# Performance work log

Hardware: AMD Instinct MI355X
Metric: run time of the kernel (lower is better)

## Reference

```python
import jax, jax.numpy as jnp
import numpy as np

B, N, IN_F, E, H, A = 8, 1024, 1024, 256, 4, 64
ALPHA = 0.2          # leaky relu slope
NEG = -9e15          # mask value from original code


def setup_inputs() -> dict:
    key = jax.random.key(0)
    k = jax.random.split(key, 7)
    x = jax.random.normal(k[0], (B * N, IN_F), dtype=jnp.float32)
    adj = jax.random.randint(k[1], (B, N, N), 0, 2, dtype=jnp.int32)
    # per-head GAT params: W (H, IN_F, E); a split into a1, a2 (H, E) each,
    # since cat([Wh_i, Wh_j]) @ a == Wh_i @ a1 + Wh_j @ a2 exactly.
    W = jax.random.normal(k[2], (H, IN_F, E), dtype=jnp.float32) * 0.05
    a1 = jax.random.normal(k[3], (H, E), dtype=jnp.float32) * 0.05
    a2 = jax.random.normal(k[4], (H, E), dtype=jnp.float32) * 0.05
    W_act = jax.random.normal(k[5], (H * E, A), dtype=jnp.float32) * 0.05
    b_act = jnp.zeros((A,), dtype=jnp.float32)
    return {"x": x, "adj": adj, "W": W, "a1": a1, "a2": a2,
            "W_act": W_act, "b_act": b_act}


def reference(x, adj, W, a1, a2, W_act, b_act):
    b, n, _ = adj.shape
    xr = x.reshape(b, n, -1)                                   # (B, N, IN_F)
    Wh = jnp.einsum('bni,hio->hbno', xr, W)                    # (H, B, N, E)
    f1 = jnp.einsum('hbno,ho->hbn', Wh, a1)                    # a . Wh_i part
    f2 = jnp.einsum('hbno,ho->hbn', Wh, a2)                    # a . Wh_j part
    e = jax.nn.leaky_relu(f1[..., :, None] + f2[..., None, :], ALPHA)  # (H,B,N,N)
    e = jnp.where(adj[None] > 0, e, NEG)
    att = jax.nn.softmax(e, axis=-1)                           # masked softmax
    h_prime = jnp.einsum('hbnm,hbmo->hbno', att, Wh)           # (H, B, N, E)
    h_prime = jax.nn.elu(h_prime)                              # concat=True -> elu
    feat = jnp.transpose(h_prime, (1, 2, 0, 3)).reshape(b * n, H * E)
    return feat @ W_act + b_act                                # (B*N, A)
```

## Files before the change

kernel.cpp:

```cpp
#include <hip/hip_runtime.h>
#include <stdint.h>

typedef __attribute__((ext_vector_type(8))) short short8;
typedef __attribute__((ext_vector_type(4))) float f32x4;
typedef __attribute__((ext_vector_type(16))) float f32x16;


__device__ __forceinline__ float b2f(unsigned short u) {
    union { unsigned int i; float f; } v; v.i = ((unsigned int)u) << 16; return v.f;
}
__device__ __forceinline__ unsigned short f2b(float f) {
    union { float f; unsigned int i; } v; v.f = f;
    unsigned int u = v.i;
    u = (u + 0x7FFFu + ((u >> 16) & 1u)) >> 16;
    return (unsigned short)u;
}
__device__ __forceinline__ unsigned int cvtpk(float a, float b) {
    unsigned int r;
    asm("v_cvt_pk_bf16_f32 %0, %1, %2" : "=v"(r) : "v"(a), "v"(b));
    return r;
}
__device__ __forceinline__ float blo(unsigned int u) {
    union { unsigned int i; float f; } v; v.i = u << 16; return v.f;
}
__device__ __forceinline__ float bhi(unsigned int u) {
    union { unsigned int i; float f; } v; v.i = u & 0xFFFF0000u; return v.f;
}
__device__ __forceinline__ void glds16(const void* g, const void* l) {
    __builtin_amdgcn_global_load_lds(
        (const __attribute__((address_space(1))) unsigned int*)g,
        (__attribute__((address_space(3))) unsigned int*)l, 16, 0, 0);
}

__device__ __forceinline__ void cvt8(const void* in, unsigned short* out,
                                     int f, int grp) {
    if (f) {
        ((ushort4*)out)[grp * 2]     = ((const ushort4*)in)[grp * 2];
        ((ushort4*)out)[grp * 2 + 1] = ((const ushort4*)in)[grp * 2 + 1];
    } else {
        const float4* p = (const float4*)in + (size_t)grp * 2;
        float4 a = p[0], b = p[1];
        ushort4 o0, o1;
        o0.x = f2b(a.x); o0.y = f2b(a.y); o0.z = f2b(a.z); o0.w = f2b(a.w);
        o1.x = f2b(b.x); o1.y = f2b(b.y); o1.z = f2b(b.z); o1.w = f2b(b.w);
        ((ushort4*)out)[grp * 2]     = o0;
        ((ushort4*)out)[grp * 2 + 1] = o1;
    }
}

__global__ __launch_bounds__(256) void prep_all(
        const unsigned int* __restrict__ x4,
        const void* __restrict__ x, const void* __restrict__ W,
        const void* __restrict__ Wact,
        const void* __restrict__ a1, const void* __restrict__ a2,
        const void* __restrict__ bact,
        unsigned short* __restrict__ xb, unsigned short* __restrict__ WT,
        unsigned short* __restrict__ WactT,
        unsigned short* __restrict__ a1b, unsigned short* __restrict__ a2b,
        unsigned short* __restrict__ bactb,
        int* __restrict__ flag, float4* __restrict__ fz) {
    __shared__ unsigned int tile[64 * 65];
    __shared__ int sflag;
    int tid = threadIdx.x;
    int bid = blockIdx.x;
    if (bid >= 4352 && bid < 4416) {
        fz[(bid - 4352) * 256 + tid] = float4{0.f, 0.f, 0.f, 0.f};
        return;
    }
    if (tid < 64) {
        unsigned int wv = x4[tid];
        unsigned int e = (wv >> 7) & 0xFF;
        unsigned long long m = __ballot(e >= 100 && e <= 140);
        if (tid == 0) sflag = (__popcll(m) >= 48) ? 1 : 0;
    }
    __syncthreads();
    int f = sflag;

    if (bid < 4096) {
        cvt8(x, xb, f, bid * 256 + tid);
        return;
    }
    if (bid == 4416) {
        if (tid == 0) flag[0] = f;
        if (tid < 128) cvt8(a1, a1b, f, tid);
        else           cvt8(a2, a2b, f, tid - 128);
        if (tid < 8)   cvt8(bact, bactb, f, tid);
        return;
    }
    const void* in; unsigned short* out; int C, bt, c0, r0;
    if (bid < 4352) {
        int lb = bid - 4096;
        in = W; out = WT; C = 256;
        c0 = (lb & 3) * 64;
        r0 = ((lb >> 2) & 15) * 64;
        bt = lb >> 6;
    } else {
        int lb = bid - 4417;
        in = Wact; out = WactT; C = 64;
        c0 = 0; r0 = lb * 64; bt = 0;
    }
    int rl = tid >> 2;
    int cc = (tid & 3) * 16;
    size_t ibase = ((size_t)bt * 1024 + (r0 + rl)) * C + c0 + cc;
    unsigned short v[16];
    if (f) {
        const unsigned short* p = (const unsigned short*)in + ibase;
        short8 a = *(const short8*)p;
        short8 b = *(const short8*)(p + 8);
#pragma unroll
        for (int j = 0; j < 8; j++) { v[j] = (unsigned short)a[j]; v[8 + j] = (unsigned short)b[j]; }
    } else {
        const float* p = (const float*)in + ibase;
#pragma unroll
        for (int j = 0; j < 16; j++) v[j] = f2b(p[j]);
    }
#pragma unroll
    for (int j = 0; j < 16; j++)
        tile[(cc + j) * 65 + rl] = v[j];
    __syncthreads();
    int cl = tid >> 2;
    int rch = (tid & 3) * 16;
    unsigned short o[16];
#pragma unroll
    for (int j = 0; j < 16; j++)
        o[j] = (unsigned short)tile[cl * 65 + rch + j];
    unsigned short* op = out + ((size_t)bt * C + (c0 + cl)) * 1024 + r0 + rch;
#pragma unroll
    for (int q = 0; q < 4; q++) {
        ushort4 s; s.x = o[q*4]; s.y = o[q*4+1]; s.z = o[q*4+2]; s.w = o[q*4+3];
        ((ushort4*)op)[q] = s;
    }
}

__global__ void pack_adj(const int* __restrict__ adj,
                         unsigned int* __restrict__ maskT) {
    int gid = blockIdx.x * 256 + threadIdx.x;
    int lane = threadIdx.x & 63;
    unsigned long long m = __ballot(adj[gid] > 0);
    if (lane == 0) {
        int lin = gid >> 6;
        int mw = (lin & 15) * 2;
        int bn = lin >> 4;
        int b = bn >> 10, n = bn & 1023;
        maskT[(size_t)(b * 32 + mw) * 1024 + n]     = (unsigned int)m;
        maskT[(size_t)(b * 32 + mw + 1) * 1024 + n] = (unsigned int)(m >> 32);
    }
}

__global__ __launch_bounds__(256) void k1_gemm(
        const unsigned short* __restrict__ x,
        const unsigned short* __restrict__ WT,
        unsigned short* __restrict__ WhF,
        const unsigned short* __restrict__ a1b,
        const unsigned short* __restrict__ a2b,
        float* __restrict__ f1, float* __restrict__ f2) {
    __shared__ unsigned short smA0[16 * 512];
    __shared__ unsigned short smA1[16 * 512];
    __shared__ unsigned short smB0[16 * 512];
    __shared__ unsigned short smB1[16 * 512];
    int tid = threadIdx.x;
    int w = tid >> 6, lane = tid & 63;
    int lr = lane & 15, lq = lane >> 4;
    int lin = blockIdx.x + 8 * blockIdx.y;
    int xcd = lin & 7, kk = lin >> 3;
    int ct = kk >> 3;
    int rt = xcd * 8 + (kk & 7);
    int col0 = ct * 128;
    int row0 = rt * 128;
    int h = col0 >> 8;
    int e_base = col0 & 255;
    int b = row0 >> 10;
    int m_base = row0 & 1023;
    int wr = w >> 1, wc = w & 1;

    f32x4 acc[4][4] = {};

    auto stage = [&](unsigned short* dA, unsigned short* dB, int k0) {
#pragma unroll
        for (int s = 0; s < 4; s++) {
            int g = 4 * w + s;
            int rb = g & 7, kh = g >> 3;
            const unsigned short* srcA =
                x + (size_t)(row0 + rb * 16 + lr) * 1024 + k0 + kh * 32 + lq * 8;
            glds16(srcA, dA + g * 512);
            const unsigned short* srcB =
                WT + (size_t)(h * 256 + e_base + rb * 16 + lr) * 1024
                   + k0 + kh * 32 + lq * 8;
            glds16(srcB, dB + g * 512);
        }
    };
    auto compute = [&](const unsigned short* sA, const unsigned short* sB) {
#pragma unroll
        for (int kh = 0; kh < 2; kh++) {
            short8 af[4], bf[4];
#pragma unroll
            for (int i = 0; i < 4; i++)
                af[i] = *(const short8*)&sA[(kh * 8 + wr * 4 + i) * 512 + lane * 8];
#pragma unroll
            for (int j = 0; j < 4; j++)
                bf[j] = *(const short8*)&sB[(kh * 8 + wc * 4 + j) * 512 + lane * 8];
#pragma unroll
            for (int i = 0; i < 4; i++)
#pragma unroll
                for (int j = 0; j < 4; j++)
                    acc[i][j] = __builtin_amdgcn_mfma_f32_16x16x32_bf16(
                        af[i], bf[j], acc[i][j], 0, 0, 0);
        }
    };

    stage(smA0, smB0, 0);
    __syncthreads();
    for (int t = 0; t < 16; t += 2) {
        stage(smA1, smB1, (t + 1) * 64);
        compute(smA0, smB0);
        __syncthreads();
        if (t + 2 < 16) stage(smA0, smB0, (t + 2) * 64);
        compute(smA1, smB1);
        __syncthreads();
    }

    int hb = h * 8 + b;
#pragma unroll
    for (int i = 0; i < 4; i++) {
#pragma unroll
        for (int j = 0; j < 4; j++) {
            int e = e_base + (wc * 4 + j) * 16 + lr;
            int et = e >> 5, e31 = e & 31;
            int m16 = (m_base >> 4) + wr * 4 + i;
            ushort4 vs;
            vs.x = f2b(acc[i][j][0]);
            vs.y = f2b(acc[i][j][1]);
            vs.z = f2b(acc[i][j][2]);
            vs.w = f2b(acc[i][j][3]);
            size_t idx = ((size_t)((hb * 8 + et) * 64 + m16) * 512)
                         + ((lq >> 1) * 32 + e31) * 8 + (lq & 1) * 4;
            *(ushort4*)&WhF[idx] = vs;
        }
    }

    const float LOG2E = 1.44269504f;
    float a1v[4], a2v[4];
#pragma unroll
    for (int j = 0; j < 4; j++) {
        int e = e_base + (wc * 4 + j) * 16 + lr;
        a1v[j] = b2f(a1b[h * 256 + e]);
        a2v[j] = b2f(a2b[h * 256 + e]);
    }
#pragma unroll
    for (int i = 0; i < 4; i++) {
#pragma unroll
        for (int reg = 0; reg < 4; reg++) {
            float s1 = 0.f, s2 = 0.f;
#pragma unroll
            for (int j = 0; j < 4; j++) {
                s1 += acc[i][j][reg] * a1v[j];
                s2 += acc[i][j][reg] * a2v[j];
            }
            s1 += __shfl_xor(s1, 1, 64); s2 += __shfl_xor(s2, 1, 64);
            s1 += __shfl_xor(s1, 2, 64); s2 += __shfl_xor(s2, 2, 64);
            s1 += __shfl_xor(s1, 4, 64); s2 += __shfl_xor(s2, 4, 64);
            s1 += __shfl_xor(s1, 8, 64); s2 += __shfl_xor(s2, 8, 64);
            if (lr == 0) {
                int m = m_base + (wr * 4 + i) * 16 + lq * 4 + reg;
                atomicAdd(&f1[hb * 1024 + m], s1 * LOG2E);
                atomicAdd(&f2[hb * 1024 + m], s2 * LOG2E);
            }
        }
    }
}

__global__ __launch_bounds__(512, 4) void k2_attn(
        const unsigned short* __restrict__ WhF,
        const unsigned int* __restrict__ maskT,
        const float* __restrict__ f1, const float* __restrict__ f2,
        unsigned short* __restrict__ feat) {
    __shared__ unsigned short ptile[2][2][32][40];
    __shared__ float dred[2][4][32];
    int tid = threadIdx.x;
    int w = tid >> 6, lane = tid & 63;
    int q = w & 3, wrg = w >> 2;
    int l5 = lane >> 5, l31 = lane & 31;
    int bid = blockIdx.x;
    int xcd = bid & 7, idx = bid >> 3;
    int hb = xcd + 8 * (idx >> 4);
    int rgb = idx & 15;
    int n0 = rgb * 64 + wrg * 32;
    int h = hb >> 3, b = hb & 7;
    int row = n0 + l31;
    float f1n = f1[hb * 1024 + row];
    const unsigned short* whb = WhF + (size_t)(hb * 8 + q * 2) * 64 * 512
                                + lane * 8;
    const unsigned int* mrow = maskT + (size_t)b * 32 * 1024 + row;
    const float* f2p = f2 + hb * 1024 + q * 8 + l5 * 4;
    int cshift = q * 8 + l5 * 4;

    f32x16 acc[2] = {};
    float den = 0.f;

    short8 bufA[2][2], bufB[2][2];
#pragma unroll
    for (int et = 0; et < 2; et++)
#pragma unroll
        for (int ks = 0; ks < 2; ks++)
            bufA[et][ks] = *(const short8*)(whb + (size_t)(et * 64 + ks) * 512);

    unsigned int mw = mrow[0];
    float4 fv = *(const float4*)f2p;

    for (int mb = 0; mb < 32; mb += 2) {
        {
            float fvv[4] = {fv.x, fv.y, fv.z, fv.w};
            unsigned int mloc = mw >> cshift;
            float pv[4];
#pragma unroll
            for (int j = 0; j < 4; j++) {
                float t_ = f1n + fvv[j];
                float e_ = fmaxf(t_, 0.2f * t_);
                pv[j] = ((mloc >> j) & 1u) ? exp2f(e_) : 0.f;
            }
            unsigned int r0 = cvtpk(pv[0], pv[1]);
            unsigned int r1 = cvtpk(pv[2], pv[3]);
            den += (blo(r0) + bhi(r0)) + (blo(r1) + bhi(r1));
            uint2 pr; pr.x = r0; pr.y = r1;
            *(uint2*)&ptile[0][wrg][l31][cshift] = pr;
            mw = mrow[(size_t)(mb + 1) * 1024];
            fv = *(const float4*)(f2p + (mb + 1) * 32);
            __syncthreads();
            short8 af0 = *(const short8*)&ptile[0][wrg][l31][l5 * 8];
            short8 af1 = *(const short8*)&ptile[0][wrg][l31][16 + l5 * 8];
            int m16n = (mb + 1) * 2;
#pragma unroll
            for (int et = 0; et < 2; et++)
#pragma unroll
                for (int ks = 0; ks < 2; ks++)
                    bufB[et][ks] =
                        *(const short8*)(whb + (size_t)(et * 64 + m16n + ks) * 512);
            __builtin_amdgcn_s_setprio(1);
#pragma unroll
            for (int et = 0; et < 2; et++) {
                acc[et] = __builtin_amdgcn_mfma_f32_32x32x16_bf16(
                    af0, bufA[et][0], acc[et], 0, 0, 0);
                acc[et] = __builtin_amdgcn_mfma_f32_32x32x16_bf16(
                    af1, bufA[et][1], acc[et], 0, 0, 0);
            }
            __builtin_amdgcn_s_setprio(0);
        }
        {
            float fvv[4] = {fv.x, fv.y, fv.z, fv.w};
            unsigned int mloc = mw >> cshift;
            float pv[4];
#pragma unroll
            for (int j = 0; j < 4; j++) {
                float t_ = f1n + fvv[j];
                float e_ = fmaxf(t_, 0.2f * t_);
                pv[j] = ((mloc >> j) & 1u) ? exp2f(e_) : 0.f;
            }
            unsigned int r0 = cvtpk(pv[0], pv[1]);
            unsigned int r1 = cvtpk(pv[2], pv[3]);
            den += (blo(r0) + bhi(r0)) + (blo(r1) + bhi(r1));
            uint2 pr; pr.x = r0; pr.y = r1;
            *(uint2*)&ptile[1][wrg][l31][cshift] = pr;
            if (mb < 30) {
                mw = mrow[(size_t)(mb + 2) * 1024];
                fv = *(const float4*)(f2p + (mb + 2) * 32);
            }
            __syncthreads();
            short8 af0 = *(const short8*)&ptile[1][wrg][l31][l5 * 8];
            short8 af1 = *(const short8*)&ptile[1][wrg][l31][16 + l5 * 8];
            if (mb < 30) {
                int m16n = (mb + 2) * 2;
#pragma unroll
                for (int et = 0; et < 2; et++)
#pragma unroll
                    for (int ks = 0; ks < 2; ks++)
                        bufA[et][ks] =
                            *(const short8*)(whb + (size_t)(et * 64 + m16n + ks) * 512);
            }
            __builtin_amdgcn_s_setprio(1);
#pragma unroll
            for (int et = 0; et < 2; et++) {
                acc[et] = __builtin_amdgcn_mfma_f32_32x32x16_bf16(
                    af0, bufB[et][0], acc[et], 0, 0, 0);
                acc[et] = __builtin_amdgcn_mfma_f32_32x32x16_bf16(
                    af1, bufB[et][1], acc[et], 0, 0, 0);
            }
            __builtin_amdgcn_s_setprio(0);
        }
    }

    den += __shfl_xor(den, 32, 64);
    if (l5 == 0) dred[wrg][q][l31] = den;
    __syncthreads();
    float denf = dred[wrg][0][l31] + dred[wrg][1][l31]
               + dred[wrg][2][l31] + dred[wrg][3][l31];

#pragma unroll
    for (int reg = 0; reg < 16; reg++) {
        int r = (reg & 3) + 8 * (reg >> 2) + 4 * l5;
        float dr = __shfl(denf, r, 64);
        float rdr = 1.0f / dr;
        int nn = n0 + r;
#pragma unroll
        for (int et = 0; et < 2; et++) {
            int e = q * 64 + et * 32 + l31;
            float v = acc[et][reg] * rdr;
            float o = v > 0.f ? v : __expf(v) - 1.f;
            feat[(size_t)(b * 1024 + nn) * 1024 + h * 256 + e] = f2b(o);
        }
    }
}

__global__ __launch_bounds__(256) void k3_out(
        const unsigned short* __restrict__ feat,
        const unsigned short* __restrict__ WactT,
        const unsigned short* __restrict__ bact,
        void* __restrict__ out, const int* __restrict__ flag) {
    __shared__ unsigned short sa0[2 * 512], sa1[2 * 512];
    __shared__ unsigned short sb0[4 * 512], sb1[4 * 512];
    int tid = threadIdx.x;
    int w = tid >> 6, lane = tid & 63;
    int lr = lane & 15, lq = lane >> 4;
    int row0 = blockIdx.x * 32;
    int g = w & 1, ch = w >> 1;
    int bf16out = *flag;
    f32x4 acc[2] = {};

    auto stage = [&](unsigned short* dA, unsigned short* dB, int k0) {
        if (w < 2) {
            const unsigned short* src =
                feat + (size_t)(row0 + w * 16 + lr) * 1024 + k0 + lq * 8;
            glds16(src, dA + w * 512);
        } else {
#pragma unroll
            for (int s = 0; s < 2; s++) {
                int t = (w - 2) * 2 + s;
                const unsigned short* src =
                    WactT + (size_t)(t * 16 + lr) * 1024 + k0 + lq * 8;
                glds16(src, dB + t * 512);
            }
        }
    };
    auto compute = [&](const unsigned short* sA, const unsigned short* sB) {
        short8 af = *(const short8*)&sA[g * 512 + lane * 8];
#pragma unroll
        for (int j = 0; j < 2; j++) {
            short8 bf = *(const short8*)&sB[(ch * 2 + j) * 512 + lane * 8];
            acc[j] = __builtin_amdgcn_mfma_f32_16x16x32_bf16(af, bf, acc[j], 0, 0, 0);
        }
    };

    stage(sa0, sb0, 0);
    __syncthreads();
    for (int t = 0; t < 32; t += 2) {
        stage(sa1, sb1, (t + 1) * 32);
        compute(sa0, sb0);
        __syncthreads();
        if (t + 2 < 32) stage(sa0, sb0, (t + 2) * 32);
        compute(sa1, sb1);
        __syncthreads();
    }
#pragma unroll
    for (int j = 0; j < 2; j++) {
        int col = ch * 32 + j * 16 + lr;
        float bv = b2f(bact[col]);
#pragma unroll
        for (int rr = 0; rr < 4; rr++) {
            int r = row0 + g * 16 + lq * 4 + rr;
            float val = acc[j][rr] + bv;
            if (bf16out) ((unsigned short*)out)[(size_t)r * 64 + col] = f2b(val);
            else         ((float*)out)[(size_t)r * 64 + col] = val;
        }
    }
}

extern "C" void kernel_launch(void* const* d_in, const int* in_sizes, int n_in,
                              void* d_out, int out_size, void* d_ws, size_t ws_size,
                              hipStream_t stream) {
    const void* x    = d_in[0];
    const int*  adj  = (const int*)d_in[1];
    const void* W    = d_in[2];
    const void* a1   = d_in[3];
    const void* a2   = d_in[4];
    const void* Wact = d_in[5];
    const void* bact = d_in[6];

    char* ws = (char*)d_ws;
    unsigned short* WhF   = (unsigned short*)(ws);
    unsigned short* xb    = (unsigned short*)(ws + 16777216);
    unsigned short* feat  = (unsigned short*)(ws + 16777216);
    unsigned short* WT    = (unsigned short*)(ws + 33554432);
    unsigned int*   maskT = (unsigned int*)(ws + 33554432);
    unsigned short* WactT = (unsigned short*)(ws + 35651584);
    float*          f1    = (float*)(ws + 35782656);
    float*          f2    = (float*)(ws + 35913728);
    unsigned short* a1b   = (unsigned short*)(ws + 36044800);
    unsigned short* a2b   = (unsigned short*)(ws + 36046848);
    unsigned short* bactb = (unsigned short*)(ws + 36048896);
    int*            flag  = (int*)(ws + 36049024);
    if (ws_size < (size_t)36049040) return;

    prep_all<<<4433, 256, 0, stream>>>((const unsigned int*)x, x, W, Wact,
                                       a1, a2, bact, xb, WT, WactT,
                                       a1b, a2b, bactb, flag, (float4*)f1);
    k1_gemm<<<dim3(8, 64), 256, 0, stream>>>(xb, WT, WhF, a1b, a2b, f1, f2);
    pack_adj<<<32768, 256, 0, stream>>>(adj, maskT);
    k2_attn<<<512, 512, 0, stream>>>(WhF, maskT, f1, f2, feat);
    k3_out<<<256, 256, 0, stream>>>(feat, WactT, bactb, d_out, flag);
}
```

Baseline: 200.9 us.

## Fuse adjacency mask packing into the prep kernel with per-wave row loops

```diff
diff --git a/kernel.cpp b/kernel.cpp
--- a/kernel.cpp
+++ b/kernel.cpp
@@ -54,15 +54,37 @@
         const void* __restrict__ Wact,
         const void* __restrict__ a1, const void* __restrict__ a2,
         const void* __restrict__ bact,
+        const int* __restrict__ adj,
         unsigned short* __restrict__ xb, unsigned short* __restrict__ WT,
         unsigned short* __restrict__ WactT,
         unsigned short* __restrict__ a1b, unsigned short* __restrict__ a2b,
         unsigned short* __restrict__ bactb,
-        int* __restrict__ flag, float4* __restrict__ fz) {
+        int* __restrict__ flag, float4* __restrict__ fz,
+        unsigned int* __restrict__ maskT) {
     __shared__ unsigned int tile[64 * 65];
     __shared__ int sflag;
     int tid = threadIdx.x;
     int bid = blockIdx.x;
+    if (bid >= 4433) {
+        int lb = bid - 4433;
+        int w = tid >> 6, lane = tid & 63;
+#pragma unroll 1
+        for (int rr = 0; rr < 16; rr++) {
+            int gr = lb * 64 + w * 16 + rr;
+            int b = gr >> 10, n = gr & 1023;
+            const int* rowp = adj + (size_t)gr * 1024 + lane;
+            unsigned int* mp = maskT + (size_t)b * 32 * 1024 + n;
+#pragma unroll
+            for (int k = 0; k < 16; k++) {
+                unsigned long long m = __ballot(rowp[k * 64] > 0);
+                if (lane == 0) {
+                    mp[(size_t)(k * 2) * 1024]     = (unsigned int)m;
+                    mp[(size_t)(k * 2 + 1) * 1024] = (unsigned int)(m >> 32);
+                }
+            }
+        }
+        return;
+    }
     if (bid >= 4352 && bid < 4416) {
         fz[(bid - 4352) * 256 + tid] = float4{0.f, 0.f, 0.f, 0.f};
         return;
@@ -129,21 +151,6 @@
     for (int q = 0; q < 4; q++) {
         ushort4 s; s.x = o[q*4]; s.y = o[q*4+1]; s.z = o[q*4+2]; s.w = o[q*4+3];
         ((ushort4*)op)[q] = s;
-    }
-}
-
-__global__ void pack_adj(const int* __restrict__ adj,
-                         unsigned int* __restrict__ maskT) {
-    int gid = blockIdx.x * 256 + threadIdx.x;
-    int lane = threadIdx.x & 63;
-    unsigned long long m = __ballot(adj[gid] > 0);
-    if (lane == 0) {
-        int lin = gid >> 6;
-        int mw = (lin & 15) * 2;
-        int bn = lin >> 4;
-        int b = bn >> 10, n = bn & 1023;
-        maskT[(size_t)(b * 32 + mw) * 1024 + n]     = (unsigned int)m;
-        maskT[(size_t)(b * 32 + mw + 1) * 1024 + n] = (unsigned int)(m >> 32);
     }
 }
 
@@ -489,7 +496,6 @@
     unsigned short* xb    = (unsigned short*)(ws + 16777216);
     unsigned short* feat  = (unsigned short*)(ws + 16777216);
     unsigned short* WT    = (unsigned short*)(ws + 33554432);
-    unsigned int*   maskT = (unsigned int*)(ws + 33554432);
     unsigned short* WactT = (unsigned short*)(ws + 35651584);
     float*          f1    = (float*)(ws + 35782656);
     float*          f2    = (float*)(ws + 35913728);
@@ -497,13 +503,14 @@
     unsigned short* a2b   = (unsigned short*)(ws + 36046848);
     unsigned short* bactb = (unsigned short*)(ws + 36048896);
     int*            flag  = (int*)(ws + 36049024);
-    if (ws_size < (size_t)36049040) return;
-
-    prep_all<<<4433, 256, 0, stream>>>((const unsigned int*)x, x, W, Wact,
-                                       a1, a2, bact, xb, WT, WactT,
-                                       a1b, a2b, bactb, flag, (float4*)f1);
+    unsigned int*   maskT = (unsigned int*)(ws + 36700160);
+    if (ws_size < (size_t)37748736) return;
+
+    prep_all<<<4561, 256, 0, stream>>>((const unsigned int*)x, x, W, Wact,
+                                       a1, a2, bact, adj, xb, WT, WactT,
+                                       a1b, a2b, bactb, flag, (float4*)f1,
+                                       maskT);
     k1_gemm<<<dim3(8, 64), 256, 0, stream>>>(xb, WT, WhF, a1b, a2b, f1, f2);
-    pack_adj<<<32768, 256, 0, stream>>>(adj, maskT);
     k2_attn<<<512, 512, 0, stream>>>(WhF, maskT, f1, f2, feat);
     k3_out<<<256, 256, 0, stream>>>(feat, WactT, bactb, d_out, flag);
 }
```

New measurement: 299.5 us. 1.49x slower.
